# Kernel optimization log

Hardware: AMD Instinct MI355X
Metric: run time of the kernel (lower is better)

## Reference

```python
import jax, jax.numpy as jnp
import numpy as np
from jax import lax

K = 8  # dct_kernel_size

def _dct_matrix(n):
    m = np.zeros((n, n), dtype=np.float32)
    for k in range(n):
        for t in range(n):
            if k == 0:
                m[k, t] = 1.0 / np.sqrt(n)
            else:
                m[k, t] = np.sqrt(2.0 / n) * np.cos(np.pi * k * (2 * t + 1) / (2.0 * n))
    return jnp.asarray(m)

DCT = _dct_matrix(K)  # [8,8]


def setup_inputs() -> dict:
    key = jax.random.key(0)
    k1, k2, k3, k4, k5 = jax.random.split(key, 5)
    x = jax.random.normal(k1, (16, 1, 512, 512), dtype=jnp.float32)
    w1 = jax.random.normal(k2, (16, 1, 3, 3), dtype=jnp.float32) * 0.1
    b1 = jax.random.normal(k3, (16,), dtype=jnp.float32) * 0.01
    w2 = jax.random.normal(k4, (32, 16, 3, 3), dtype=jnp.float32) * 0.1
    b2 = jax.random.normal(k5, (32,), dtype=jnp.float32) * 0.01
    return {"x": x, "w1": w1, "b1": b1, "w2": w2, "b2": b2}


def _conv(x, w, b):
    y = lax.conv_general_dilated(x, w, (1, 1), 'SAME',
                                 dimension_numbers=('NCHW', 'OIHW', 'NCHW'))
    return y + b[None, :, None, None]


def reference(x, w1, b1, w2, b2):
    B, _, H, W = x.shape
    # non-overlapping 8x8 patches (equivalent to F.unfold k=stride=8)
    p = x.reshape(B, H // K, K, W // K, K).transpose(0, 1, 3, 2, 4)
    p = p.reshape(-1, K, K)                       # [P, 8, 8]
    # 2D DCT: DCT @ p @ DCT^T
    c = jnp.einsum('ij,pjk,lk->pil', DCT, p, DCT)  # [P, 8, 8]
    c = c[:, None]                                 # [P, 1, 8, 8]
    h = jax.nn.relu(_conv(c, w1, b1))              # [P, 16, 8, 8]
    h = _conv(h, w2, b2)                           # [P, 32, 8, 8]
    v = h.mean(axis=(2, 3))                        # adaptive avg pool -> [P, 32]
    C = v.shape[-1]
    return v.reshape(B, -1, C).mean(axis=1)        # [B, 32]
```

## Files before the change

### kernel.cpp

```cpp
#include <hip/hip_runtime.h>

namespace {

constexpr int NIMG = 16;
constexpr int C1N  = 16;
constexpr int C2N  = 32;
constexpr int PART = C1N * 9;

typedef __attribute__((ext_vector_type(8)))  _Float16 half8;
typedef __attribute__((ext_vector_type(16))) float    f32x16;

__device__ const float DCTM[8][8] = {
  {0.35355339059327373f, 0.35355339059327373f, 0.35355339059327373f, 0.35355339059327373f,
   0.35355339059327373f, 0.35355339059327373f, 0.35355339059327373f, 0.35355339059327373f},
  {0.49039264020161522f, 0.41573480615127262f, 0.27778511650980111f, 0.09754516100806413f,
  -0.09754516100806413f,-0.27778511650980111f,-0.41573480615127262f,-0.49039264020161522f},
  {0.46193976625564337f, 0.19134171618254492f,-0.19134171618254492f,-0.46193976625564337f,
  -0.46193976625564337f,-0.19134171618254492f, 0.19134171618254492f, 0.46193976625564337f},
  {0.41573480615127262f,-0.09754516100806413f,-0.49039264020161522f,-0.27778511650980111f,
   0.27778511650980111f, 0.49039264020161522f, 0.09754516100806413f,-0.41573480615127262f},
  {0.35355339059327373f,-0.35355339059327373f,-0.35355339059327373f, 0.35355339059327373f,
   0.35355339059327373f,-0.35355339059327373f,-0.35355339059327373f, 0.35355339059327373f},
  {0.27778511650980111f,-0.49039264020161522f, 0.09754516100806413f, 0.41573480615127262f,
  -0.41573480615127262f,-0.09754516100806413f, 0.49039264020161522f,-0.27778511650980111f},
  {0.19134171618254492f,-0.46193976625564337f, 0.46193976625564337f,-0.19134171618254492f,
  -0.19134171618254492f, 0.46193976625564337f,-0.46193976625564337f, 0.19134171618254492f},
  {0.09754516100806413f,-0.27778511650980111f, 0.41573480615127262f,-0.49039264020161522f,
   0.49039264020161522f,-0.41573480615127262f, 0.27778511650980111f,-0.09754516100806413f},
};

__global__ __launch_bounds__(256) void setup_M(
    const float* __restrict__ w1, const float* __restrict__ b1,
    _Float16* __restrict__ Mf)
{
  const int f = blockIdx.x * 256 + threadIdx.x;
  if (f >= 32 * 5 * 64) return;
  const int l  = f & 63;
  const int rc = f >> 6;
  const int c  = rc % 5;
  const int rt = rc / 5;
  const int ch = rt >> 1;
  const int hi = l >> 5;
  const int s  = (rt & 1) * 32 + (l & 31);
  const int i = s >> 3, j = s & 7;

  half8 e;
  if (c == 4) {
    #pragma unroll
    for (int b = 0; b < 8; ++b) e[b] = (_Float16)0.f;
    if (hi == 0) e[0] = (_Float16)b1[ch];
  } else {
    #pragma unroll
    for (int b = 0; b < 8; ++b) {
      const int k = c * 16 + hi * 8 + b;
      const int u = k >> 3, v = k & 7;
      float acc = 0.f;
      for (int di = 0; di < 3; ++di) {
        const int ii = i + di - 1;
        if (ii < 0 || ii > 7) continue;
        for (int dj = 0; dj < 3; ++dj) {
          const int jj = j + dj - 1;
          if (jj < 0 || jj > 7) continue;
          acc = fmaf(w1[ch * 9 + di * 3 + dj], DCTM[ii][u] * DCTM[jj][v], acc);
        }
      }
      e[b] = (_Float16)acc;
    }
  }
  *reinterpret_cast<half8*>(Mf + (size_t)f * 8) = e;
}

__global__ __launch_bounds__(64, 2) void gemm_kernel(
    const float* __restrict__ x, const _Float16* __restrict__ Mf,
    float* __restrict__ partials)
{
  const int bid   = blockIdx.x;
  const int slice = bid >> 9;
  const int g     = bid & 511;
  const int img   = g >> 5, gi = g & 31;
  const int lane  = threadIdx.x;
  const int col   = lane & 31, hi = lane >> 5;

  half8 bfrag[4][4];
  #pragma unroll
  for (int ct = 0; ct < 4; ++ct) {
    const int prow = 2 * gi + (ct >> 1);
    const int pcol = (ct & 1) * 32 + col;
    const float* pb = x + (((size_t)img * 512 + (size_t)prow * 8) * 512 + (size_t)pcol * 8);
    #pragma unroll
    for (int m = 0; m < 4; ++m) {
      const int u = 2 * m + hi;
      const float4 lo = *reinterpret_cast<const float4*>(pb + (size_t)u * 512);
      const float4 h4 = *reinterpret_cast<const float4*>(pb + (size_t)u * 512 + 4);
      half8 h;
      h[0] = (_Float16)lo.x; h[1] = (_Float16)lo.y; h[2] = (_Float16)lo.z; h[3] = (_Float16)lo.w;
      h[4] = (_Float16)h4.x; h[5] = (_Float16)h4.y; h[6] = (_Float16)h4.z; h[7] = (_Float16)h4.w;
      bfrag[ct][m] = h;
    }
  }
  const float hm0 = (hi == 0) ? 1.f : 0.f;
  const float hm1 = 1.f - hm0;
  half8 bones;
  #pragma unroll
  for (int b = 0; b < 8; ++b) bones[b] = (_Float16)0.f;
  bones[0] = (_Float16)hm0;

  #pragma unroll 1
  for (int cc = 0; cc < 4; ++cc) {
    float t_ = 0.f, r0 = 0.f, r7 = 0.f, c0 = 0.f, c7 = 0.f;
    float k00 = 0.f, k07 = 0.f, k70 = 0.f, k77 = 0.f;
    #pragma unroll
    for (int rp = 0; rp < 2; ++rp) {
      const int rtg = slice * 8 + cc * 2 + rp;
      const _Float16* ap = Mf + ((size_t)(rtg * 5) * 64 + (size_t)lane) * 8;
      const half8 a0 = *reinterpret_cast<const half8*>(ap);
      const half8 a1 = *reinterpret_cast<const half8*>(ap + 512);
      const half8 a2 = *reinterpret_cast<const half8*>(ap + 1024);
      const half8 a3 = *reinterpret_cast<const half8*>(ap + 1536);
      const half8 a4 = *reinterpret_cast<const half8*>(ap + 2048);
      #pragma unroll
      for (int ct = 0; ct < 4; ++ct) {
        f32x16 d;
        #pragma unroll
        for (int r = 0; r < 16; ++r) d[r] = 0.f;
        d = __builtin_amdgcn_mfma_f32_32x32x16_f16(a0, bfrag[ct][0], d, 0, 0, 0);
        d = __builtin_amdgcn_mfma_f32_32x32x16_f16(a1, bfrag[ct][1], d, 0, 0, 0);
        d = __builtin_amdgcn_mfma_f32_32x32x16_f16(a2, bfrag[ct][2], d, 0, 0, 0);
        d = __builtin_amdgcn_mfma_f32_32x32x16_f16(a3, bfrag[ct][3], d, 0, 0, 0);
        d = __builtin_amdgcn_mfma_f32_32x32x16_f16(a4, bones,        d, 0, 0, 0);

        float v[16];
        #pragma unroll
        for (int r = 0; r < 16; ++r) v[r] = fmaxf(d[r], 0.f);
        const float q0 = (v[0]  + v[1])  + (v[2]  + v[3]);
        const float q1 = (v[4]  + v[5])  + (v[6]  + v[7]);
        const float q2 = (v[8]  + v[9])  + (v[10] + v[11]);
        const float q3 = (v[12] + v[13]) + (v[14] + v[15]);
        t_ += (q0 + q1) + (q2 + q3);
        if (rp == 0) {
          r0 += q0;
          k00 = fmaf(hm0, v[0],  k00);
          k07 = fmaf(hm1, v[3],  k07);
        } else {
          r7 += q3;
          k70 = fmaf(hm0, v[12], k70);
          k77 = fmaf(hm1, v[15], k77);
        }
        c0 = fmaf(hm0, (v[0] + v[4]) + (v[8]  + v[12]), c0);
        c7 = fmaf(hm1, (v[3] + v[7]) + (v[11] + v[15]), c7);
      }
    }
    float vv[9] = {t_, r0, r7, c0, c7, k00, k07, k70, k77};
    #pragma unroll
    for (int q = 0; q < 9; ++q) {
      float s = vv[q];
      s += __shfl_xor(s, 1); s += __shfl_xor(s, 2);
      s += __shfl_xor(s, 4); s += __shfl_xor(s, 8);
      vv[q] = s;
    }
    if ((lane & 15) == 0) {
      const size_t prw = (size_t)g * 4 + (lane >> 4);
      float* dst = partials + prw * PART + (size_t)(slice * 4 + cc) * 9;
      #pragma unroll
      for (int q = 0; q < 9; ++q) dst[q] = vv[q];
    }
  }
}

__global__ __launch_bounds__(576) void finish_kernel(
    const float* __restrict__ w2, const float* __restrict__ b2,
    const float* __restrict__ partials, float* __restrict__ out)
{
  const int img  = blockIdx.x;
  const int tid  = threadIdx.x;
  const int comp = tid % PART;
  const int chnk = tid / PART;

  __shared__ float part[4][PART];
  __shared__ float acc[C1N][9];

  {
    float s = 0.f;
    const float* pb = partials + ((size_t)img * 128 + (size_t)chnk * 32) * PART + comp;
    for (int k = 0; k < 32; ++k) s += pb[(size_t)k * PART];
    part[chnk][comp] = s;
  }
  __syncthreads();
  if (tid < PART) {
    acc[tid / 9][tid % 9] = (part[0][tid] + part[1][tid]) + (part[2][tid] + part[3][tid]);
  }
  __syncthreads();
  if (tid < C2N) {
    float r = 0.f;
    for (int c1 = 0; c1 < C1N; ++c1) {
      const float T  = acc[c1][0], R0 = acc[c1][1], R7 = acc[c1][2];
      const float Q0 = acc[c1][3], Q7 = acc[c1][4];
      const float K00 = acc[c1][5], K07 = acc[c1][6], K70 = acc[c1][7], K77 = acc[c1][8];
      const float* wp = w2 + (size_t)(tid * C1N + c1) * 9;
      #pragma unroll
      for (int di = 0; di < 3; ++di) {
        #pragma unroll
        for (int dj = 0; dj < 3; ++dj) {
          float S = T;
          if (di == 0) S -= R7;
          if (di == 2) S -= R0;
          if (dj == 0) S -= Q7;
          if (dj == 2) S -= Q0;
          if (di == 0 && dj == 0) S += K77;
          if (di == 0 && dj == 2) S += K70;
          if (di == 2 && dj == 0) S += K07;
          if (di == 2 && dj == 2) S += K00;
          r = fmaf(wp[di * 3 + dj], S, r);
        }
      }
    }
    out[img * C2N + tid] = b2[tid] + r * (1.0f / 262144.0f);
  }
}

}

extern "C" void kernel_launch(void* const* d_in, const int* in_sizes, int n_in,
                              void* d_out, int out_size, void* d_ws, size_t ws_size,
                              hipStream_t stream) {
  const float* x  = (const float*)d_in[0];
  const float* w1 = (const float*)d_in[1];
  const float* b1 = (const float*)d_in[2];
  const float* w2 = (const float*)d_in[3];
  const float* b2 = (const float*)d_in[4];
  float* out      = (float*)d_out;

  _Float16* Mf    = (_Float16*)d_ws;
  float* partials = (float*)((char*)d_ws + 262144);

  setup_M<<<40, 256, 0, stream>>>(w1, b1, Mf);
  gemm_kernel<<<2048, 64, 0, stream>>>(x, Mf, partials);
  finish_kernel<<<NIMG, 576, 0, stream>>>(w2, b2, partials, out);
}
```

Baseline: 31.55 us.

## Map channel slices to waves within a block, one patch row per block

Restructures the GEMM launch so that each 256-thread block handles one patch row of one image, with its four waves covering the four channel slices. Previously each 64-thread block handled two patch rows for a single slice. The intent is to have the slices' x reads for the same patch row land close together in time, improving cache reuse, and to halve the per-wave B fragments, which lowers register pressure. In exchange, the partials buffer grows to 256 rows per image, so the finish kernel reads twice as many partial rows.

```diff
diff --git a/kernel.cpp b/kernel.cpp
--- a/kernel.cpp
+++ b/kernel.cpp
@@ -70,22 +70,21 @@
   *reinterpret_cast<half8*>(Mf + (size_t)f * 8) = e;
 }
 
-__global__ __launch_bounds__(64, 2) void gemm_kernel(
+__global__ __launch_bounds__(256, 4) void gemm_kernel(
     const float* __restrict__ x, const _Float16* __restrict__ Mf,
     float* __restrict__ partials)
 {
-  const int bid   = blockIdx.x;
-  const int slice = bid >> 9;
-  const int g     = bid & 511;
-  const int img   = g >> 5, gi = g & 31;
-  const int lane  = threadIdx.x;
+  const int b     = blockIdx.x;
+  const int img   = b >> 6;
+  const int prow  = b & 63;
+  const int lane  = threadIdx.x & 63;
+  const int slice = threadIdx.x >> 6;
   const int col   = lane & 31, hi = lane >> 5;
 
-  half8 bfrag[4][4];
+  half8 bfrag[2][4];
   #pragma unroll
-  for (int ct = 0; ct < 4; ++ct) {
-    const int prow = 2 * gi + (ct >> 1);
-    const int pcol = (ct & 1) * 32 + col;
+  for (int ctl = 0; ctl < 2; ++ctl) {
+    const int pcol = ctl * 32 + col;
     const float* pb = x + (((size_t)img * 512 + (size_t)prow * 8) * 512 + (size_t)pcol * 8);
     #pragma unroll
     for (int m = 0; m < 4; ++m) {
@@ -95,14 +94,14 @@
       half8 h;
       h[0] = (_Float16)lo.x; h[1] = (_Float16)lo.y; h[2] = (_Float16)lo.z; h[3] = (_Float16)lo.w;
       h[4] = (_Float16)h4.x; h[5] = (_Float16)h4.y; h[6] = (_Float16)h4.z; h[7] = (_Float16)h4.w;
-      bfrag[ct][m] = h;
+      bfrag[ctl][m] = h;
     }
   }
   const float hm0 = (hi == 0) ? 1.f : 0.f;
   const float hm1 = 1.f - hm0;
   half8 bones;
   #pragma unroll
-  for (int b = 0; b < 8; ++b) bones[b] = (_Float16)0.f;
+  for (int q = 0; q < 8; ++q) bones[q] = (_Float16)0.f;
   bones[0] = (_Float16)hm0;
 
   #pragma unroll 1
@@ -119,15 +118,15 @@
       const half8 a3 = *reinterpret_cast<const half8*>(ap + 1536);
       const half8 a4 = *reinterpret_cast<const half8*>(ap + 2048);
       #pragma unroll
-      for (int ct = 0; ct < 4; ++ct) {
+      for (int ctl = 0; ctl < 2; ++ctl) {
         f32x16 d;
         #pragma unroll
         for (int r = 0; r < 16; ++r) d[r] = 0.f;
-        d = __builtin_amdgcn_mfma_f32_32x32x16_f16(a0, bfrag[ct][0], d, 0, 0, 0);
-        d = __builtin_amdgcn_mfma_f32_32x32x16_f16(a1, bfrag[ct][1], d, 0, 0, 0);
-        d = __builtin_amdgcn_mfma_f32_32x32x16_f16(a2, bfrag[ct][2], d, 0, 0, 0);
-        d = __builtin_amdgcn_mfma_f32_32x32x16_f16(a3, bfrag[ct][3], d, 0, 0, 0);
-        d = __builtin_amdgcn_mfma_f32_32x32x16_f16(a4, bones,        d, 0, 0, 0);
+        d = __builtin_amdgcn_mfma_f32_32x32x16_f16(a0, bfrag[ctl][0], d, 0, 0, 0);
+        d = __builtin_amdgcn_mfma_f32_32x32x16_f16(a1, bfrag[ctl][1], d, 0, 0, 0);
+        d = __builtin_amdgcn_mfma_f32_32x32x16_f16(a2, bfrag[ctl][2], d, 0, 0, 0);
+        d = __builtin_amdgcn_mfma_f32_32x32x16_f16(a3, bfrag[ctl][3], d, 0, 0, 0);
+        d = __builtin_amdgcn_mfma_f32_32x32x16_f16(a4, bones,         d, 0, 0, 0);
 
         float v[16];
         #pragma unroll
@@ -159,7 +158,7 @@
       vv[q] = s;
     }
     if ((lane & 15) == 0) {
-      const size_t prw = (size_t)g * 4 + (lane >> 4);
+      const size_t prw = (size_t)b * 4 + (lane >> 4);
       float* dst = partials + prw * PART + (size_t)(slice * 4 + cc) * 9;
       #pragma unroll
       for (int q = 0; q < 9; ++q) dst[q] = vv[q];
@@ -175,14 +174,16 @@
   const int tid  = threadIdx.x;
   const int comp = tid % PART;
   const int chnk = tid / PART;
+  constexpr int ROWS = 256;
+  constexpr int RPC  = ROWS / 4;
 
   __shared__ float part[4][PART];
   __shared__ float acc[C1N][9];
 
   {
     float s = 0.f;
-    const float* pb = partials + ((size_t)img * 128 + (size_t)chnk * 32) * PART + comp;
-    for (int k = 0; k < 32; ++k) s += pb[(size_t)k * PART];
+    const float* pb = partials + ((size_t)img * ROWS + (size_t)chnk * RPC) * PART + comp;
+    for (int k = 0; k < RPC; ++k) s += pb[(size_t)k * PART];
     part[chnk][comp] = s;
   }
   __syncthreads();
@@ -234,6 +235,6 @@
   float* partials = (float*)((char*)d_ws + 262144);
 
   setup_M<<<40, 256, 0, stream>>>(w1, b1, Mf);
-  gemm_kernel<<<2048, 64, 0, stream>>>(x, Mf, partials);
+  gemm_kernel<<<1024, 256, 0, stream>>>(x, Mf, partials);
   finish_kernel<<<NIMG, 576, 0, stream>>>(w2, b2, partials, out);
 }
```

Result: slower. 39.01 us (+23.7%).

## Fold conv1 bias into accumulator init and split channels across two waves

Applied to the files above, without the earlier changes.

The bias MFMA against a ones fragment is removed. Each accumulator is now initialised with the b1 value, so the GEMM drops from five MFMAs per tile to four and the A matrix shrinks. The block grows to two waves, each handling half of a slice's channels, which doubles the number of waves in flight for latency hiding. The cost is that each wave reloads and converts the same x patches, doubling global and L2 traffic for the input.

```diff
diff --git a/kernel.cpp b/kernel.cpp
--- a/kernel.cpp
+++ b/kernel.cpp
@@ -30,55 +30,50 @@
 };
 
 __global__ __launch_bounds__(256) void setup_M(
-    const float* __restrict__ w1, const float* __restrict__ b1,
-    _Float16* __restrict__ Mf)
+    const float* __restrict__ w1, _Float16* __restrict__ Mf)
 {
   const int f = blockIdx.x * 256 + threadIdx.x;
-  if (f >= 32 * 5 * 64) return;
+  if (f >= 32 * 4 * 64) return;
   const int l  = f & 63;
   const int rc = f >> 6;
-  const int c  = rc % 5;
-  const int rt = rc / 5;
+  const int c  = rc & 3;
+  const int rt = rc >> 2;
   const int ch = rt >> 1;
   const int hi = l >> 5;
   const int s  = (rt & 1) * 32 + (l & 31);
   const int i = s >> 3, j = s & 7;
 
   half8 e;
-  if (c == 4) {
-    #pragma unroll
-    for (int b = 0; b < 8; ++b) e[b] = (_Float16)0.f;
-    if (hi == 0) e[0] = (_Float16)b1[ch];
-  } else {
-    #pragma unroll
-    for (int b = 0; b < 8; ++b) {
-      const int k = c * 16 + hi * 8 + b;
-      const int u = k >> 3, v = k & 7;
-      float acc = 0.f;
-      for (int di = 0; di < 3; ++di) {
-        const int ii = i + di - 1;
-        if (ii < 0 || ii > 7) continue;
-        for (int dj = 0; dj < 3; ++dj) {
-          const int jj = j + dj - 1;
-          if (jj < 0 || jj > 7) continue;
-          acc = fmaf(w1[ch * 9 + di * 3 + dj], DCTM[ii][u] * DCTM[jj][v], acc);
-        }
+  #pragma unroll
+  for (int b = 0; b < 8; ++b) {
+    const int k = c * 16 + hi * 8 + b;
+    const int u = k >> 3, v = k & 7;
+    float acc = 0.f;
+    for (int di = 0; di < 3; ++di) {
+      const int ii = i + di - 1;
+      if (ii < 0 || ii > 7) continue;
+      for (int dj = 0; dj < 3; ++dj) {
+        const int jj = j + dj - 1;
+        if (jj < 0 || jj > 7) continue;
+        acc = fmaf(w1[ch * 9 + di * 3 + dj], DCTM[ii][u] * DCTM[jj][v], acc);
       }
-      e[b] = (_Float16)acc;
-    }
+    }
+    e[b] = (_Float16)acc;
   }
   *reinterpret_cast<half8*>(Mf + (size_t)f * 8) = e;
 }
 
-__global__ __launch_bounds__(64, 2) void gemm_kernel(
+__global__ __launch_bounds__(128, 4) void gemm_kernel(
     const float* __restrict__ x, const _Float16* __restrict__ Mf,
-    float* __restrict__ partials)
+    const float* __restrict__ b1, float* __restrict__ partials)
 {
   const int bid   = blockIdx.x;
-  const int slice = bid >> 9;
   const int g     = bid & 511;
+  const int hs    = ((bid >> 9) << 1) | (threadIdx.x >> 6);
+  const int slice = hs >> 1;
+  const int chp   = hs & 1;
   const int img   = g >> 5, gi = g & 31;
-  const int lane  = threadIdx.x;
+  const int lane  = threadIdx.x & 63;
   const int col   = lane & 31, hi = lane >> 5;
 
   half8 bfrag[4][4];
@@ -100,34 +95,30 @@
   }
   const float hm0 = (hi == 0) ? 1.f : 0.f;
   const float hm1 = 1.f - hm0;
-  half8 bones;
-  #pragma unroll
-  for (int b = 0; b < 8; ++b) bones[b] = (_Float16)0.f;
-  bones[0] = (_Float16)hm0;
 
   #pragma unroll 1
-  for (int cc = 0; cc < 4; ++cc) {
+  for (int cc = 0; cc < 2; ++cc) {
+    const int chl = chp * 2 + cc;
+    const float bb = b1[slice * 4 + chl];
     float t_ = 0.f, r0 = 0.f, r7 = 0.f, c0 = 0.f, c7 = 0.f;
     float k00 = 0.f, k07 = 0.f, k70 = 0.f, k77 = 0.f;
     #pragma unroll
     for (int rp = 0; rp < 2; ++rp) {
-      const int rtg = slice * 8 + cc * 2 + rp;
-      const _Float16* ap = Mf + ((size_t)(rtg * 5) * 64 + (size_t)lane) * 8;
+      const int rtg = slice * 8 + chl * 2 + rp;
+      const _Float16* ap = Mf + ((size_t)(rtg * 4) * 64 + (size_t)lane) * 8;
       const half8 a0 = *reinterpret_cast<const half8*>(ap);
       const half8 a1 = *reinterpret_cast<const half8*>(ap + 512);
       const half8 a2 = *reinterpret_cast<const half8*>(ap + 1024);
       const half8 a3 = *reinterpret_cast<const half8*>(ap + 1536);
-      const half8 a4 = *reinterpret_cast<const half8*>(ap + 2048);
       #pragma unroll
       for (int ct = 0; ct < 4; ++ct) {
         f32x16 d;
         #pragma unroll
-        for (int r = 0; r < 16; ++r) d[r] = 0.f;
+        for (int r = 0; r < 16; ++r) d[r] = bb;
         d = __builtin_amdgcn_mfma_f32_32x32x16_f16(a0, bfrag[ct][0], d, 0, 0, 0);
         d = __builtin_amdgcn_mfma_f32_32x32x16_f16(a1, bfrag[ct][1], d, 0, 0, 0);
         d = __builtin_amdgcn_mfma_f32_32x32x16_f16(a2, bfrag[ct][2], d, 0, 0, 0);
         d = __builtin_amdgcn_mfma_f32_32x32x16_f16(a3, bfrag[ct][3], d, 0, 0, 0);
-        d = __builtin_amdgcn_mfma_f32_32x32x16_f16(a4, bones,        d, 0, 0, 0);
 
         float v[16];
         #pragma unroll
@@ -160,7 +151,7 @@
     }
     if ((lane & 15) == 0) {
       const size_t prw = (size_t)g * 4 + (lane >> 4);
-      float* dst = partials + prw * PART + (size_t)(slice * 4 + cc) * 9;
+      float* dst = partials + prw * PART + (size_t)(slice * 4 + chl) * 9;
       #pragma unroll
       for (int q = 0; q < 9; ++q) dst[q] = vv[q];
     }
@@ -175,14 +166,16 @@
   const int tid  = threadIdx.x;
   const int comp = tid % PART;
   const int chnk = tid / PART;
+  constexpr int ROWS = 128;
+  constexpr int RPC  = ROWS / 4;
 
   __shared__ float part[4][PART];
   __shared__ float acc[C1N][9];
 
   {
     float s = 0.f;
-    const float* pb = partials + ((size_t)img * 128 + (size_t)chnk * 32) * PART + comp;
-    for (int k = 0; k < 32; ++k) s += pb[(size_t)k * PART];
+    const float* pb = partials + ((size_t)img * ROWS + (size_t)chnk * RPC) * PART + comp;
+    for (int k = 0; k < RPC; ++k) s += pb[(size_t)k * PART];
     part[chnk][comp] = s;
   }
   __syncthreads();
@@ -233,7 +226,7 @@
   _Float16* Mf    = (_Float16*)d_ws;
   float* partials = (float*)((char*)d_ws + 262144);
 
-  setup_M<<<40, 256, 0, stream>>>(w1, b1, Mf);
-  gemm_kernel<<<2048, 64, 0, stream>>>(x, Mf, partials);
+  setup_M<<<32, 256, 0, stream>>>(w1, Mf);
+  gemm_kernel<<<2048, 128, 0, stream>>>(x, Mf, b1, partials);
   finish_kernel<<<NIMG, 576, 0, stream>>>(w2, b2, partials, out);
 }
```

Result: slower. 90.42 us (+186.6%).
